# Performance work log

Measured on AMD Instinct MI355X. Metric: run time of the kernel, lower is better.

Reference implementation:

```python
import jax, jax.numpy as jnp
import numpy as np

B, IN, H = 4096, 1024, 4096
EPS = 1e-5

def setup_inputs() -> dict:
    key = jax.random.key(0)
    ks = jax.random.split(key, 20)
    std = 0.01
    inp = {
        "input": jax.random.normal(ks[0], (B, IN), jnp.float32),
        "max_v": jnp.ones((1,), jnp.float32),
        "min_v": jnp.zeros((1,), jnp.float32),
        "hidden": jax.random.normal(ks[1], (B, 1, H), jnp.float32),
        "Wr_w": std * jax.random.normal(ks[2], (H, IN), jnp.float32),
        "Wr_b": std * jax.random.normal(ks[3], (H,), jnp.float32),
        "Ur_w": std * jax.random.normal(ks[4], (H, H), jnp.float32),
        "Ur_b": std * jax.random.normal(ks[5], (H,), jnp.float32),
        "Wz_w": std * jax.random.normal(ks[6], (H, IN), jnp.float32),
        "Wz_b": std * jax.random.normal(ks[7], (H,), jnp.float32),
        "Uz_w": std * jax.random.normal(ks[8], (H, H), jnp.float32),
        "Uz_b": std * jax.random.normal(ks[9], (H,), jnp.float32),
        "Wh_w": std * jax.random.normal(ks[10], (H, IN), jnp.float32),
        "Wh_b": std * jax.random.normal(ks[11], (H,), jnp.float32),
        "Uh_w": std * jax.random.normal(ks[12], (H, H), jnp.float32),
        "Uh_b": std * jax.random.normal(ks[13], (H,), jnp.float32),
        "out_w": std * jax.random.normal(ks[14], (4, H), jnp.float32),
        "out_b": std * jax.random.normal(ks[15], (4,), jnp.float32),
        "bn_gamma": jnp.ones((1,), jnp.float32),
        "bn_beta": jnp.zeros((1,), jnp.float32),
    }
    return inp

def _lin(x, W, b):
    # x: [B,1,F], W: [O,F] -> [B,1,O]
    return jnp.einsum('blf,of->blo', x, W) + b

def reference(input, max_v, min_v, hidden, Wr_w, Wr_b, Ur_w, Ur_b, Wz_w, Wz_b,
              Uz_w, Uz_b, Wh_w, Wh_b, Uh_w, Uh_b, out_w, out_b, bn_gamma, bn_beta):
    x = input[:, None, :]  # [B,1,IN]
    reset_gate = jax.nn.sigmoid(_lin(x, Wr_w, Wr_b) + _lin(hidden, Ur_w, Ur_b))
    update_gate = jax.nn.sigmoid(_lin(x, Wz_w, Wz_b) + _lin(hidden, Uz_w, Uz_b))
    h_pre = _lin(x, Wh_w, Wh_b) + reset_gate * _lin(hidden, Uh_w, Uh_b)  # [B,1,H]
    # BatchNorm1d(1) in training mode: single channel -> normalize over ALL elements
    mean = jnp.mean(h_pre)
    var = jnp.mean(jnp.square(h_pre - mean))  # biased variance (torch norm uses biased)
    h_bn = (h_pre - mean) * jax.lax.rsqrt(var + EPS) * bn_gamma[0] + bn_beta[0]
    proposal = jax.nn.relu(h_bn)
    current_state = (1.0 - update_gate) * hidden + update_gate * proposal  # [B,1,H]
    out = jnp.einsum('blh,oh->blo', current_state, out_w) + out_b  # [B,1,4]
    return (current_state, out[:, :, 0], out[:, :, 1], out[:, :, 2], out[:, :, 3])
```

## Files before the change

kernel.cpp:

```cpp
#include <hip/hip_runtime.h>

#define HH 4096
#define BB 4096
#define IND 1024
#define NTOT 16777216
#define EPSV 1e-5f

typedef unsigned short u16;
typedef __bf16 bf16x8 __attribute__((ext_vector_type(8)));
typedef float f32x4 __attribute__((ext_vector_type(4)));
typedef u16 u16x8 __attribute__((ext_vector_type(8)));

__device__ __forceinline__ u16 f2bf(float f) {
    unsigned u = __builtin_bit_cast(unsigned, f);
    u += 0x7fffu + ((u >> 16) & 1u);
    return (u16)(u >> 16);
}
__device__ __forceinline__ float bf2f(u16 h) {
    return __builtin_bit_cast(float, ((unsigned)h) << 16);
}

__global__ void cvt_kernel(const float* __restrict__ src, u16* __restrict__ dst, int n) {
    int i4 = (blockIdx.x * blockDim.x + threadIdx.x) * 4;
    int stride = gridDim.x * blockDim.x * 4;
    for (; i4 < n; i4 += stride) {
        f32x4 v = *(const f32x4*)(src + i4);
        u16 o0 = f2bf(v[0]), o1 = f2bf(v[1]), o2 = f2bf(v[2]), o3 = f2bf(v[3]);
        unsigned p0 = (unsigned)o0 | ((unsigned)o1 << 16);
        unsigned p1 = (unsigned)o2 | ((unsigned)o3 << 16);
        *(uint2*)(dst + i4) = make_uint2(p0, p1);
    }
}


__device__ __forceinline__ void stage_tile(const u16* __restrict__ g, int ld, int row0, int k0,
                                           u16* lds, int tid) {
    const int l = tid & 63, w = tid >> 6;
#pragma unroll
    for (int j = 0; j < 4; ++j) {
        const int sub = j * 4 + w;
        const int d = l << 4;
        const int lin = d ^ (((d >> 9) & 1) << 5);
        const int r = ((sub >> 1) << 4) | (lin >> 6);
        const int c = ((sub & 1) << 5) | ((lin & 63) >> 1);
        const u16* ga = g + (size_t)(row0 + r) * ld + (k0 + c);
        __builtin_amdgcn_global_load_lds(
            (const __attribute__((address_space(1))) unsigned*)ga,
            (__attribute__((address_space(3))) unsigned*)(lds + (sub << 9)),
            16, 0, 0);
    }
}

__device__ __forceinline__ void zero_acc(f32x4 (&acc)[4][4]) {
#pragma unroll
    for (int i = 0; i < 4; ++i)
#pragma unroll
        for (int j = 0; j < 4; ++j) {
            f32x4 zz = {0.f, 0.f, 0.f, 0.f};
            acc[i][j] = zz;
        }
}

__device__ __forceinline__ void run_phase(const u16* __restrict__ A, int row0a,
                                          const u16* __restrict__ B, int ld, int Klen,
                                          u16* Alds, u16* Blds,
                                          f32x4 (&acc)[4][4], int tid) {
    const int l = tid & 63;
    const int wid = tid >> 6;
    const int wr = wid >> 1, wc = wid & 1;
    const int lr = l & 15, lq = l >> 4;
    const int swzh = (((lr << 6) | (lq << 4)) ^ ((lr & 8) << 2)) >> 1;
    for (int k0 = 0; k0 < Klen; k0 += 64) {
        stage_tile(A, ld, row0a, k0, Alds, tid);
        stage_tile(B, ld, 0, k0, Blds, tid);
        __syncthreads();
#pragma unroll
        for (int kk = 0; kk < 2; ++kk) {
            bf16x8 af[4], bfr[4];
#pragma unroll
            for (int i = 0; i < 4; ++i)
                af[i] = *(const bf16x8*)(Alds + ((wr * 8 + i * 2 + kk) << 9) + swzh);
#pragma unroll
            for (int j = 0; j < 4; ++j)
                bfr[j] = *(const bf16x8*)(Blds + ((wc * 8 + j * 2 + kk) << 9) + swzh);
#pragma unroll
            for (int i = 0; i < 4; ++i)
#pragma unroll
                for (int j = 0; j < 4; ++j)
                    acc[i][j] = __builtin_amdgcn_mfma_f32_16x16x32_bf16(af[i], bfr[j], acc[i][j], 0, 0, 0);
        }
        __syncthreads();
    }
}

__global__ __launch_bounds__(256, 2) void gru_gemm(
    const u16* __restrict__ xbf, const u16* __restrict__ hbf,
    const u16* __restrict__ Wr, const u16* __restrict__ Ur,
    const u16* __restrict__ Wz, const u16* __restrict__ Uz,
    const u16* __restrict__ Wh, const u16* __restrict__ Uh,
    const float* __restrict__ Wr_b, const float* __restrict__ Ur_b,
    const float* __restrict__ Wz_b, const float* __restrict__ Uz_b,
    const float* __restrict__ Wh_b, const float* __restrict__ Uh_b,
    u16* __restrict__ z_out, u16* __restrict__ hpre_out, float* __restrict__ partials) {
    __shared__ __align__(16) u16 Alds[128 * 64];
    __shared__ __align__(16) u16 Blds[128 * 64];
    __shared__ float redS[4], redSS[4];

    const int tid = threadIdx.x;
    const int bid = blockIdx.x;
    const int wg = (bid & 7) * 128 + (bid >> 3);
    const int m0 = (wg & 31) * 128, n0 = (wg >> 5) * 128;
    const int l = tid & 63, wid = tid >> 6;
    const int wr = wid >> 1, wc = wid & 1;

    f32x4 acc[4][4];

    zero_acc(acc);
    run_phase(xbf, m0, Wr + (size_t)n0 * IND, IND, IND, Alds, Blds, acc, tid);
    run_phase(hbf, m0, Ur + (size_t)n0 * HH, HH, HH, Alds, Blds, acc, tid);

    float r_st[4][4][4];
#pragma unroll
    for (int j = 0; j < 4; ++j) {
        int col = n0 + wc * 64 + j * 16 + (l & 15);
        float bias = __ldg(Wr_b + col) + __ldg(Ur_b + col);
#pragma unroll
        for (int i = 0; i < 4; ++i)
#pragma unroll
            for (int q = 0; q < 4; ++q)
                r_st[i][j][q] = 1.f / (1.f + __expf(-(acc[i][j][q] + bias)));
    }

    zero_acc(acc);
    run_phase(xbf, m0, Wz + (size_t)n0 * IND, IND, IND, Alds, Blds, acc, tid);
    run_phase(hbf, m0, Uz + (size_t)n0 * HH, HH, HH, Alds, Blds, acc, tid);
#pragma unroll
    for (int j = 0; j < 4; ++j) {
        int col = n0 + wc * 64 + j * 16 + (l & 15);
        float bias = __ldg(Wz_b + col) + __ldg(Uz_b + col);
#pragma unroll
        for (int i = 0; i < 4; ++i) {
            int rowb = m0 + wr * 64 + i * 16 + (l >> 4) * 4;
#pragma unroll
            for (int q = 0; q < 4; ++q) {
                float zv = 1.f / (1.f + __expf(-(acc[i][j][q] + bias)));
                z_out[(size_t)(rowb + q) * HH + col] = f2bf(zv);
            }
        }
    }

    zero_acc(acc);
    run_phase(hbf, m0, Uh + (size_t)n0 * HH, HH, HH, Alds, Blds, acc, tid);
#pragma unroll
    for (int j = 0; j < 4; ++j) {
        int col = n0 + wc * 64 + j * 16 + (l & 15);
        float bias = __ldg(Uh_b + col);
#pragma unroll
        for (int i = 0; i < 4; ++i)
#pragma unroll
            for (int q = 0; q < 4; ++q)
                acc[i][j][q] = r_st[i][j][q] * (acc[i][j][q] + bias);
    }
    run_phase(xbf, m0, Wh + (size_t)n0 * IND, IND, IND, Alds, Blds, acc, tid);

    float s = 0.f, ss = 0.f;
#pragma unroll
    for (int j = 0; j < 4; ++j) {
        int col = n0 + wc * 64 + j * 16 + (l & 15);
        float bias = __ldg(Wh_b + col);
#pragma unroll
        for (int i = 0; i < 4; ++i) {
            int rowb = m0 + wr * 64 + i * 16 + (l >> 4) * 4;
#pragma unroll
            for (int q = 0; q < 4; ++q) {
                float hv = acc[i][j][q] + bias;
                hpre_out[(size_t)(rowb + q) * HH + col] = f2bf(hv);
                s += hv;
                ss += hv * hv;
            }
        }
    }
#pragma unroll
    for (int off = 32; off; off >>= 1) {
        s += __shfl_down(s, off, 64);
        ss += __shfl_down(ss, off, 64);
    }
    if (l == 0) { redS[wid] = s; redSS[wid] = ss; }
    __syncthreads();
    if (tid == 0) {
        partials[2 * bid] = redS[0] + redS[1] + redS[2] + redS[3];
        partials[2 * bid + 1] = redSS[0] + redSS[1] + redSS[2] + redSS[3];
    }
}

__global__ void reduce_stats(const float* __restrict__ partials, int nblk,
                             const float* __restrict__ gamma, const float* __restrict__ beta,
                             float* __restrict__ stats) {
    __shared__ float rs[4], rss[4];
    int tid = threadIdx.x;
    float s = 0.f, ss = 0.f;
    for (int i = tid; i < nblk; i += blockDim.x) {
        s += partials[2 * i];
        ss += partials[2 * i + 1];
    }
#pragma unroll
    for (int off = 32; off; off >>= 1) {
        s += __shfl_down(s, off, 64);
        ss += __shfl_down(ss, off, 64);
    }
    if ((tid & 63) == 0) { rs[tid >> 6] = s; rss[tid >> 6] = ss; }
    __syncthreads();
    if (tid == 0) {
        float S = rs[0] + rs[1] + rs[2] + rs[3];
        float SS = rss[0] + rss[1] + rss[2] + rss[3];
        float mean = S / (float)NTOT;
        float var = SS / (float)NTOT - mean * mean;
        float scale = gamma[0] * rsqrtf(var + EPSV);
        stats[0] = scale;
        stats[1] = beta[0] - mean * scale;
    }
}

__global__ __launch_bounds__(256) void finalize(
    const u16* __restrict__ z, const u16* __restrict__ hpre,
    const float* __restrict__ hidden, const float* __restrict__ out_w,
    const float* __restrict__ out_b, const float* __restrict__ stats,
    float* __restrict__ d_out) {
    __shared__ float red[4][4];
    const int b = blockIdx.x, t = threadIdx.x;
    const float scale = stats[0], shift = stats[1];
    const size_t row = (size_t)b * HH;
    float so[4] = {0.f, 0.f, 0.f, 0.f};
#pragma unroll
    for (int jj = 0; jj < 2; ++jj) {
        int h0 = jj * 2048 + t * 8;
        u16x8 zv = *(const u16x8*)(z + row + h0);
        u16x8 hp = *(const u16x8*)(hpre + row + h0);
        f32x4 hd0 = *(const f32x4*)(hidden + row + h0);
        f32x4 hd1 = *(const f32x4*)(hidden + row + h0 + 4);
        f32x4 o0, o1;
#pragma unroll
        for (int e = 0; e < 8; ++e) {
            float zf = bf2f(zv[e]);
            float pv = bf2f(hp[e]) * scale + shift;
            pv = pv > 0.f ? pv : 0.f;
            float hf = (e < 4) ? hd0[e] : hd1[e - 4];
            float cs = (1.f - zf) * hf + zf * pv;
            if (e < 4) o0[e] = cs; else o1[e - 4] = cs;
#pragma unroll
            for (int o = 0; o < 4; ++o)
                so[o] += cs * __ldg(out_w + o * HH + h0 + e);
        }
        *(f32x4*)(d_out + row + h0) = o0;
        *(f32x4*)(d_out + row + h0 + 4) = o1;
    }
#pragma unroll
    for (int off = 32; off; off >>= 1)
#pragma unroll
        for (int o = 0; o < 4; ++o) so[o] += __shfl_down(so[o], off, 64);
    if ((t & 63) == 0)
#pragma unroll
        for (int o = 0; o < 4; ++o) red[t >> 6][o] = so[o];
    __syncthreads();
    if (t < 4) {
        float v = red[0][t] + red[1][t] + red[2][t] + red[3][t] + __ldg(out_b + t);
        d_out[(size_t)NTOT + (size_t)t * BB + b] = v;
    }
}

extern "C" void kernel_launch(void* const* d_in, const int* in_sizes, int n_in,
                              void* d_out, int out_size, void* d_ws, size_t ws_size,
                              hipStream_t stream) {
    const float* input = (const float*)d_in[0];
    const float* hidden = (const float*)d_in[3];
    const float* Wr_w = (const float*)d_in[4];  const float* Wr_b = (const float*)d_in[5];
    const float* Ur_w = (const float*)d_in[6];  const float* Ur_b = (const float*)d_in[7];
    const float* Wz_w = (const float*)d_in[8];  const float* Wz_b = (const float*)d_in[9];
    const float* Uz_w = (const float*)d_in[10]; const float* Uz_b = (const float*)d_in[11];
    const float* Wh_w = (const float*)d_in[12]; const float* Wh_b = (const float*)d_in[13];
    const float* Uh_w = (const float*)d_in[14]; const float* Uh_b = (const float*)d_in[15];
    const float* out_w = (const float*)d_in[16]; const float* out_b = (const float*)d_in[17];
    const float* gamma = (const float*)d_in[18]; const float* beta = (const float*)d_in[19];

    char* ws = (char*)d_ws;
    size_t off = 0;
    auto alloc = [&](size_t bytes) {
        void* p = ws + off;
        off = (off + bytes + 255) & ~(size_t)255;
        return p;
    };
    u16* xbf = (u16*)alloc((size_t)BB * IND * 2);
    u16* hbf = (u16*)alloc((size_t)BB * HH * 2);
    u16* wr = (u16*)alloc((size_t)HH * IND * 2);
    u16* wz = (u16*)alloc((size_t)HH * IND * 2);
    u16* wh = (u16*)alloc((size_t)HH * IND * 2);
    u16* ur = (u16*)alloc((size_t)HH * HH * 2);
    u16* uz = (u16*)alloc((size_t)HH * HH * 2);
    u16* uh = (u16*)alloc((size_t)HH * HH * 2);
    u16* zpl = (u16*)alloc((size_t)BB * HH * 2);
    u16* hpl = (u16*)alloc((size_t)BB * HH * 2);
    float* partials = (float*)alloc(2048 * sizeof(float));
    float* stats = (float*)alloc(16);

    cvt_kernel<<<512, 256, 0, stream>>>(input, xbf, BB * IND);
    cvt_kernel<<<2048, 256, 0, stream>>>(hidden, hbf, BB * HH);
    cvt_kernel<<<512, 256, 0, stream>>>(Wr_w, wr, HH * IND);
    cvt_kernel<<<512, 256, 0, stream>>>(Wz_w, wz, HH * IND);
    cvt_kernel<<<512, 256, 0, stream>>>(Wh_w, wh, HH * IND);
    cvt_kernel<<<2048, 256, 0, stream>>>(Ur_w, ur, HH * HH);
    cvt_kernel<<<2048, 256, 0, stream>>>(Uz_w, uz, HH * HH);
    cvt_kernel<<<2048, 256, 0, stream>>>(Uh_w, uh, HH * HH);

    gru_gemm<<<1024, 256, 0, stream>>>(xbf, hbf, wr, ur, wz, uz, wh, uh,
                                       Wr_b, Ur_b, Wz_b, Uz_b, Wh_b, Uh_b,
                                       zpl, hpl, partials);
    reduce_stats<<<1, 256, 0, stream>>>(partials, 1024, gamma, beta, stats);
    finalize<<<BB, 256, 0, stream>>>(zpl, hpl, hidden, out_w, out_b, stats, (float*)d_out);
}
```

Measured before the change: 884.9 us.

## Spill reset gate to global scratch to raise GEMM occupancy

The reset-gate tile is no longer held in registers across the Uh GEMM phase. It is written as bf16 into the output buffer, used as scratch, and read back before the Wh phase. This lowers register pressure so launch bounds can go from 2 to 4 blocks per CU, and the grid becomes a plain 2D launch in place of the swizzled 1D block mapping. The cost is extra global write and read traffic for r plus the loss of the L2-friendly block order, and the scratch aliases d_out, which finalize later overwrites.

Measured after the change: 754.7 us. 1.17x faster.

```diff
diff --git a/kernel.cpp b/kernel.cpp
--- a/kernel.cpp
+++ b/kernel.cpp
@@ -93,7 +93,7 @@
     }
 }
 
-__global__ __launch_bounds__(256, 2) void gru_gemm(
+__global__ __launch_bounds__(256, 4) void gru_gemm(
     const u16* __restrict__ xbf, const u16* __restrict__ hbf,
     const u16* __restrict__ Wr, const u16* __restrict__ Ur,
     const u16* __restrict__ Wz, const u16* __restrict__ Uz,
@@ -101,34 +101,36 @@
     const float* __restrict__ Wr_b, const float* __restrict__ Ur_b,
     const float* __restrict__ Wz_b, const float* __restrict__ Uz_b,
     const float* __restrict__ Wh_b, const float* __restrict__ Uh_b,
-    u16* __restrict__ z_out, u16* __restrict__ hpre_out, float* __restrict__ partials) {
+    u16* __restrict__ r_out, u16* __restrict__ z_out,
+    u16* __restrict__ hpre_out, float* __restrict__ partials) {
     __shared__ __align__(16) u16 Alds[128 * 64];
     __shared__ __align__(16) u16 Blds[128 * 64];
     __shared__ float redS[4], redSS[4];
 
     const int tid = threadIdx.x;
-    const int bid = blockIdx.x;
-    const int wg = (bid & 7) * 128 + (bid >> 3);
-    const int m0 = (wg & 31) * 128, n0 = (wg >> 5) * 128;
+    const int m0 = blockIdx.x * 128, n0 = blockIdx.y * 128;
     const int l = tid & 63, wid = tid >> 6;
     const int wr = wid >> 1, wc = wid & 1;
+    const int lr = l & 15, lq = l >> 4;
 
     f32x4 acc[4][4];
 
     zero_acc(acc);
     run_phase(xbf, m0, Wr + (size_t)n0 * IND, IND, IND, Alds, Blds, acc, tid);
     run_phase(hbf, m0, Ur + (size_t)n0 * HH, HH, HH, Alds, Blds, acc, tid);
-
-    float r_st[4][4][4];
-#pragma unroll
-    for (int j = 0; j < 4; ++j) {
-        int col = n0 + wc * 64 + j * 16 + (l & 15);
-        float bias = __ldg(Wr_b + col) + __ldg(Ur_b + col);
-#pragma unroll
-        for (int i = 0; i < 4; ++i)
-#pragma unroll
-            for (int q = 0; q < 4; ++q)
-                r_st[i][j][q] = 1.f / (1.f + __expf(-(acc[i][j][q] + bias)));
+#pragma unroll
+    for (int j = 0; j < 4; ++j) {
+        int col = n0 + wc * 64 + j * 16 + lr;
+        float bias = Wr_b[col] + Ur_b[col];
+#pragma unroll
+        for (int i = 0; i < 4; ++i) {
+            int rowb = m0 + wr * 64 + i * 16 + lq * 4;
+#pragma unroll
+            for (int q = 0; q < 4; ++q) {
+                float rv = 1.f / (1.f + __expf(-(acc[i][j][q] + bias)));
+                r_out[(size_t)(rowb + q) * HH + col] = f2bf(rv);
+            }
+        }
     }
 
     zero_acc(acc);
@@ -136,11 +138,11 @@
     run_phase(hbf, m0, Uz + (size_t)n0 * HH, HH, HH, Alds, Blds, acc, tid);
 #pragma unroll
     for (int j = 0; j < 4; ++j) {
-        int col = n0 + wc * 64 + j * 16 + (l & 15);
-        float bias = __ldg(Wz_b + col) + __ldg(Uz_b + col);
+        int col = n0 + wc * 64 + j * 16 + lr;
+        float bias = Wz_b[col] + Uz_b[col];
 #pragma unroll
         for (int i = 0; i < 4; ++i) {
-            int rowb = m0 + wr * 64 + i * 16 + (l >> 4) * 4;
+            int rowb = m0 + wr * 64 + i * 16 + lq * 4;
 #pragma unroll
             for (int q = 0; q < 4; ++q) {
                 float zv = 1.f / (1.f + __expf(-(acc[i][j][q] + bias)));
@@ -153,24 +155,28 @@
     run_phase(hbf, m0, Uh + (size_t)n0 * HH, HH, HH, Alds, Blds, acc, tid);
 #pragma unroll
     for (int j = 0; j < 4; ++j) {
-        int col = n0 + wc * 64 + j * 16 + (l & 15);
-        float bias = __ldg(Uh_b + col);
-#pragma unroll
-        for (int i = 0; i < 4; ++i)
-#pragma unroll
-            for (int q = 0; q < 4; ++q)
-                acc[i][j][q] = r_st[i][j][q] * (acc[i][j][q] + bias);
+        int col = n0 + wc * 64 + j * 16 + lr;
+        float bias = Uh_b[col];
+#pragma unroll
+        for (int i = 0; i < 4; ++i) {
+            int rowb = m0 + wr * 64 + i * 16 + lq * 4;
+#pragma unroll
+            for (int q = 0; q < 4; ++q) {
+                float rv = bf2f(r_out[(size_t)(rowb + q) * HH + col]);
+                acc[i][j][q] = rv * (acc[i][j][q] + bias);
+            }
+        }
     }
     run_phase(xbf, m0, Wh + (size_t)n0 * IND, IND, IND, Alds, Blds, acc, tid);
 
     float s = 0.f, ss = 0.f;
 #pragma unroll
     for (int j = 0; j < 4; ++j) {
-        int col = n0 + wc * 64 + j * 16 + (l & 15);
-        float bias = __ldg(Wh_b + col);
+        int col = n0 + wc * 64 + j * 16 + lr;
+        float bias = Wh_b[col];
 #pragma unroll
         for (int i = 0; i < 4; ++i) {
-            int rowb = m0 + wr * 64 + i * 16 + (l >> 4) * 4;
+            int rowb = m0 + wr * 64 + i * 16 + lq * 4;
 #pragma unroll
             for (int q = 0; q < 4; ++q) {
                 float hv = acc[i][j][q] + bias;
@@ -188,6 +194,7 @@
     if (l == 0) { redS[wid] = s; redSS[wid] = ss; }
     __syncthreads();
     if (tid == 0) {
+        int bid = blockIdx.y * 32 + blockIdx.x;
         partials[2 * bid] = redS[0] + redS[1] + redS[2] + redS[3];
         partials[2 * bid + 1] = redSS[0] + redSS[1] + redSS[2] + redSS[3];
     }
@@ -302,6 +309,8 @@
     float* partials = (float*)alloc(2048 * sizeof(float));
     float* stats = (float*)alloc(16);
 
+    u16* rpl = (u16*)d_out;
+
     cvt_kernel<<<512, 256, 0, stream>>>(input, xbf, BB * IND);
     cvt_kernel<<<2048, 256, 0, stream>>>(hidden, hbf, BB * HH);
     cvt_kernel<<<512, 256, 0, stream>>>(Wr_w, wr, HH * IND);
@@ -311,9 +320,9 @@
     cvt_kernel<<<2048, 256, 0, stream>>>(Uz_w, uz, HH * HH);
     cvt_kernel<<<2048, 256, 0, stream>>>(Uh_w, uh, HH * HH);
 
-    gru_gemm<<<1024, 256, 0, stream>>>(xbf, hbf, wr, ur, wz, uz, wh, uh,
-                                       Wr_b, Ur_b, Wz_b, Uz_b, Wh_b, Uh_b,
-                                       zpl, hpl, partials);
+    gru_gemm<<<dim3(32, 32), 256, 0, stream>>>(xbf, hbf, wr, ur, wz, uz, wh, uh,
+                                               Wr_b, Ur_b, Wz_b, Uz_b, Wh_b, Uh_b,
+                                               rpl, zpl, hpl, partials);
     reduce_stats<<<1, 256, 0, stream>>>(partials, 1024, gamma, beta, stats);
     finalize<<<BB, 256, 0, stream>>>(zpl, hpl, hidden, out_w, out_b, stats, (float*)d_out);
 }
```
